# Performance work log

Measured on AMD Instinct MI355X. Metric: run time of the kernel, lower is better.

Reference implementation:

```python
import math
import jax, jax.numpy as jnp
import numpy as np

B, T, D, H, NEXP, TOPK = 2, 1024, 1024, 16, 8, 2
DH = D // H
DFF = 4 * D
NEG = -1e30


def _ln(x, g, b, eps=1e-5):
    m = jnp.mean(x, axis=-1, keepdims=True)
    v = jnp.mean((x - m) ** 2, axis=-1, keepdims=True)
    return (x - m) * jax.lax.rsqrt(v + eps) * g + b


def _build_sin_cos(t, dim, base=10000.0):
    # matches torch build_sin_cos(seq_len, head_dim//2): inv freq over range(0, dim*2, 2)
    pos = jnp.arange(t, dtype=jnp.float32)[:, None]
    inv = jnp.exp(jnp.arange(0, dim * 2, 2, dtype=jnp.float32) * (-math.log(base) / (dim * 2)))
    ang = pos * inv  # (T, dim)
    return jnp.sin(ang), jnp.cos(ang)


def _rope(q, k, sin, cos):
    half = q.shape[-1] // 2
    sin = sin[None, :, None, :]
    cos = cos[None, :, None, :]
    q1, q2 = q[..., :half], q[..., half:]
    k1, k2 = k[..., :half], k[..., half:]
    qr = jnp.concatenate([q1 * cos - q2 * sin, q2 * cos + q1 * sin], axis=-1)
    kr = jnp.concatenate([k1 * cos - k2 * sin, k2 * cos + k1 * sin], axis=-1)
    return qr, kr


def _forward(x, noise, ln1_g, ln1_b, ln2_g, ln2_b, w_qkv, w_proj, w_rl, b_rl, w_rn, b_rn, w1, b1, w2, b2):
    # ---- attention sublayer (LN -> RoPE -> causal attn -> proj, residual) ----
    h = _ln(x, ln1_g, ln1_b)
    qkv = (h @ w_qkv).reshape(B, T, 3, H, DH)
    q, k, v = qkv[:, :, 0], qkv[:, :, 1], qkv[:, :, 2]  # (B,T,H,DH)
    sin, cos = _build_sin_cos(T, DH // 2)
    q, k = _rope(q, k, sin, cos)
    scores = jnp.einsum('bthd,bshd->bhts', q, k) / math.sqrt(DH)
    causal = jnp.tril(jnp.ones((T, T), dtype=bool))
    scores = jnp.where(causal[None, None], scores, NEG)
    attn = jax.nn.softmax(scores, axis=-1)
    ao = jnp.einsum('bhts,bshd->bthd', attn, v).reshape(B, T, D)
    x = x + ao @ w_proj
    # ---- MoE sublayer (noisy top-k router -> capped expert dispatch, residual) ----
    h2 = _ln(x, ln2_g, ln2_b).reshape(B * T, D)
    nz = noise.reshape(B * T, NEXP)
    logits = h2 @ w_rl + b_rl
    noisy = logits + nz * jax.nn.softplus(h2 @ w_rn + b_rn)
    topv, ix = jax.lax.top_k(noisy, TOPK)              # (N,K)
    pk = jax.nn.softmax(topv, axis=-1)                 # softmax over sparse (-inf elsewhere)
    route_p = jnp.sum(pk[..., None] * jax.nn.one_hot(ix, NEXP, dtype=pk.dtype), axis=-2)  # (N,E)
    N = B * T
    cap = int(N * TOPK / NEXP)  # capacity per expert (cap_factor=1.0)
    updates = jnp.zeros((N, D), dtype=x.dtype)
    for i in range(NEXP):
        mask = jnp.any(ix == i, axis=-1)               # (N,) tokens routed to expert i
        sel = jnp.argsort(jnp.logical_not(mask))[:cap]  # first `cap` routed tokens, in order (stable sort)
        valid = mask[sel].astype(x.dtype)              # zero out slots beyond actual routed count
        xe = h2[sel]                                   # (cap, D)
        o = jax.nn.relu(xe @ w1[i] + b1[i]) @ w2[i] + b2[i]
        gate = route_p[sel, i] * valid
        updates = updates.at[sel].add(o * gate[:, None])
    return x + updates.reshape(B, T, D)


def setup_inputs() -> dict:
    key = jax.random.key(0)
    ks = jax.random.split(key, 8)
    s = 0.02
    return {
        'x': jax.random.normal(ks[0], (B, T, D), jnp.float32),
        'noise': jax.random.normal(ks[1], (B, T, NEXP), jnp.float32),
        'ln1_g': jnp.ones((D,), jnp.float32),
        'ln1_b': jnp.zeros((D,), jnp.float32),
        'ln2_g': jnp.ones((D,), jnp.float32),
        'ln2_b': jnp.zeros((D,), jnp.float32),
        'w_qkv': jax.random.normal(ks[2], (D, 3 * D), jnp.float32) * s,
        'w_proj': jax.random.normal(ks[3], (D, D), jnp.float32) * s,
        'w_rl': jax.random.normal(ks[4], (D, NEXP), jnp.float32) * s,
        'b_rl': jnp.zeros((NEXP,), jnp.float32),
        'w_rn': jax.random.normal(ks[5], (D, NEXP), jnp.float32) * s,
        'b_rn': jnp.zeros((NEXP,), jnp.float32),
        'w1': jax.random.normal(ks[6], (NEXP, D, DFF), jnp.float32) * s,
        'b1': jnp.zeros((NEXP, DFF), jnp.float32),
        'w2': jax.random.normal(ks[7], (NEXP, DFF, D), jnp.float32) * s,
        'b2': jnp.zeros((NEXP, D), jnp.float32),
    }


def reference(x, noise, ln1_g, ln1_b, ln2_g, ln2_b, w_qkv, w_proj, w_rl, b_rl, w_rn, b_rn, w1, b1, w2, b2):
    return _forward(x, noise, ln1_g, ln1_b, ln2_g, ln2_b, w_qkv, w_proj, w_rl, b_rl, w_rn, b_rn, w1, b1, w2, b2)
```

## Files before the change

kernel.cpp:

```cpp
#include <hip/hip_runtime.h>


#define TB 1024
#define DD 1024
#define NTOK 2048
#define NEXPERT 8
#define CAPN 512
#define DFF 4096

typedef __attribute__((ext_vector_type(4))) float f32x4;
typedef __attribute__((ext_vector_type(16))) float f32x16;
typedef __attribute__((ext_vector_type(8))) short short8;
typedef __attribute__((ext_vector_type(4))) short short4v;
typedef unsigned short u16;
typedef unsigned int u32;

__device__ __forceinline__ u16 f2bf(float f){
  union { float f; u32 u; } v; v.f = f;
  u32 u = v.u;
  u32 r = (u + 0x7fffu + ((u >> 16) & 1u)) >> 16;
  return (u16)r;
}
__device__ __forceinline__ float bf2f(u16 b){
  union { u32 u; float f; } v; v.u = ((u32)b) << 16;
  return v.f;
}
__device__ __forceinline__ float waveRedSum(float v){
#pragma unroll
  for (int o = 1; o < 64; o <<= 1) v += __shfl_xor(v, o);
  return v;
}

__device__ __forceinline__ void gl16(const u16* g, u16* l){
  __builtin_amdgcn_global_load_lds(
    (const __attribute__((address_space(1))) u32*)g,
    (__attribute__((address_space(3))) u32*)l, 16, 0, 0);
}

__global__ __launch_bounds__(256) void k_prep(
    const float* __restrict__ w_qkv, const float* __restrict__ w_proj,
    const float* __restrict__ w1, const float* __restrict__ w2,
    u16* __restrict__ wqkvT, u16* __restrict__ wprojT,
    u16* __restrict__ w1T, u16* __restrict__ w2T,
    float* __restrict__ st, float* __restrict__ ct)
{
  const int tid = threadIdx.x;
  int bid = blockIdx.x;
  if (bid < 128){
    const int idx = bid * 256 + tid;
    const int t = idx >> 5, i = idx & 31;
    const float inv = expf((float)(2 * i) * (-0.14391157f));
    const float ang = (float)t * inv;
    st[idx] = sinf(ang);
    ct[idx] = cosf(ang);
    return;
  }
  bid -= 128;
  const float* src; u16* dst; int K, N, nx, tile;
  long zoff = 0;
  if (bid < 768){
    src = w_qkv; dst = wqkvT; K = DD; N = 3*DD; nx = 48; tile = bid;
  } else if (bid < 768 + 256){
    src = w_proj; dst = wprojT; K = DD; N = DD; nx = 16; tile = bid - 768;
  } else if (bid < 768 + 256 + 8192){
    const int b2 = bid - (768 + 256);
    src = w1; dst = w1T; K = DD; N = DFF; nx = 64; tile = b2 & 1023;
    zoff = (long)(b2 >> 10) * DD * DFF;
  } else {
    const int b2 = bid - (768 + 256 + 8192);
    src = w2; dst = w2T; K = DFF; N = DD; nx = 16; tile = b2 & 1023;
    zoff = (long)(b2 >> 10) * DFF * DD;
  }
  const int n0 = (tile % nx) * 64, k0 = (tile / nx) * 64;
  __shared__ float tb[64][65];
  const int r  = tid >> 2;
  const int c4 = (tid & 3) * 16;
#pragma unroll
  for (int j = 0; j < 4; ++j){
    const float4 v = *(const float4*)(src + zoff + (long)(k0 + r)*N + n0 + c4 + j*4);
    tb[r][c4 + j*4 + 0] = v.x;
    tb[r][c4 + j*4 + 1] = v.y;
    tb[r][c4 + j*4 + 2] = v.z;
    tb[r][c4 + j*4 + 3] = v.w;
  }
  __syncthreads();
  const int n  = tid >> 2;
  const int ks = (tid & 3) * 16;
  short8 o0, o1;
#pragma unroll
  for (int j = 0; j < 8; ++j){
    o0[j] = (short)f2bf(tb[ks + j][n]);
    o1[j] = (short)f2bf(tb[ks + 8 + j][n]);
  }
  u16* dp = dst + zoff + (long)(n0 + n)*K + k0 + ks;
  *(short8*)dp = o0;
  *(short8*)(dp + 8) = o1;
}

template<bool GATHER>
__device__ __forceinline__ void gemm_core5(
    const u16* __restrict__ A, int lda, const int* __restrict__ rowlist,
    const u16* __restrict__ Bt, int ldb, int K, int kstart, int row0, int col0,
    u16* As0, u16* Bs0, u16* As1, u16* Bs1, f32x16 acc[2][2])
{
  const int tid = threadIdx.x;
  const int lane = tid & 63;
  const int w = tid >> 6;
  const int wr = w >> 1, wc = w & 1;
  const int l31 = lane & 31, l5 = lane >> 5;
  const int rr8 = lane >> 3;
  const int cc8 = ((lane & 7) ^ rr8) * 8;

  const u16* Aq[4];
  const u16* Bq[4];
  int coff[4];
#pragma unroll
  for (int j2 = 0; j2 < 4; ++j2){
    const int j = w + 4*j2;
    long ar;
    if constexpr (GATHER) ar = rowlist[row0 + j*8 + rr8];
    else                  ar = row0 + j*8 + rr8;
    Aq[j2] = A + ar*(long)lda + kstart + cc8;
    Bq[j2] = Bt + (long)(col0 + j*8 + rr8)*ldb + kstart + cc8;
    coff[j2] = j*512;
  }

  const int swz = (l31 & 7) * 8;

#define STAGE5(AS, BS, KOFF) \
  _Pragma("unroll") \
  for (int j2 = 0; j2 < 4; ++j2){ \
    gl16(Aq[j2] + (KOFF), (AS) + coff[j2]); \
    gl16(Bq[j2] + (KOFF), (BS) + coff[j2]); \
  }

#define COMPUTE5(AS, BS) \
  _Pragma("unroll") \
  for (int s = 0; s < 4; ++s){ \
    short8 aF[2], bF[2]; \
    const int cread = ((s*16 + l5*8) ^ swz); \
    _Pragma("unroll") \
    for (int mi = 0; mi < 2; ++mi) \
      aF[mi] = *(const short8*)((AS) + (wr*64 + mi*32 + l31)*64 + cread); \
    _Pragma("unroll") \
    for (int ni = 0; ni < 2; ++ni) \
      bF[ni] = *(const short8*)((BS) + (wc*64 + ni*32 + l31)*64 + cread); \
    _Pragma("unroll") \
    for (int mi = 0; mi < 2; ++mi) \
      _Pragma("unroll") \
      for (int ni = 0; ni < 2; ++ni) \
        acc[mi][ni] = __builtin_amdgcn_mfma_f32_32x32x16_bf16(aF[mi], bF[ni], acc[mi][ni], 0, 0, 0); \
  }

  STAGE5(As0, Bs0, 0)

  for (int k0 = 0; k0 < K; k0 += 128){
    STAGE5(As1, Bs1, k0 + 64)
    asm volatile("s_waitcnt vmcnt(8)" ::: "memory");
    __builtin_amdgcn_s_barrier();
    __builtin_amdgcn_sched_barrier(0);
    COMPUTE5(As0, Bs0)
    __builtin_amdgcn_s_barrier();
    if (k0 + 128 < K){
      STAGE5(As0, Bs0, k0 + 128)
      asm volatile("s_waitcnt vmcnt(8)" ::: "memory");
    } else {
      asm volatile("s_waitcnt vmcnt(0)" ::: "memory");
    }
    __builtin_amdgcn_s_barrier();
    __builtin_amdgcn_sched_barrier(0);
    COMPUTE5(As1, Bs1)
    __builtin_amdgcn_s_barrier();
  }
#undef STAGE5
#undef COMPUTE5
}

#define GEMM_PRE4 \
  __shared__ u16 As0[128*64], Bs0[128*64], As1[128*64], Bs1[128*64]; \
  f32x16 acc[2][2]; \
  _Pragma("unroll") for (int i = 0; i < 2; ++i) \
  _Pragma("unroll") for (int j = 0; j < 2; ++j) \
  _Pragma("unroll") for (int q = 0; q < 16; ++q) acc[i][j][q] = 0.f;

#define GEMM_EPI4_VARS \
  const int lane = threadIdx.x & 63; \
  const int wv = threadIdx.x >> 6;   \
  const int wr = wv >> 1, wc = wv & 1; \
  const int l31 = lane & 31, l5 = lane >> 5;

#define ROW4(mi, r) (row0 + wr*64 + (mi)*32 + ((r)&3) + (((r)>>2)<<3) + l5*4)
#define COL4(ni)    (col0 + wc*64 + (ni)*32 + l31)

__global__ __launch_bounds__(256) void k_ln(const float* __restrict__ x,
    const float* __restrict__ g, const float* __restrict__ bb,
    u16* __restrict__ hb)
{
  const int row = blockIdx.x, tid = threadIdx.x;
  const int w = tid >> 6, lane = tid & 63;
  const float4 xv = *(const float4*)(x + (long)row*DD + tid*4);
  __shared__ float red[8];
  float s = xv.x + xv.y + xv.z + xv.w;
  s = waveRedSum(s);
  if (lane == 0) red[w] = s;
  __syncthreads();
  const float mean = (red[0]+red[1]+red[2]+red[3]) * (1.f/1024.f);
  const float d0 = xv.x-mean, d1 = xv.y-mean, d2 = xv.z-mean, d3 = xv.w-mean;
  float vs = d0*d0 + d1*d1 + d2*d2 + d3*d3;
  vs = waveRedSum(vs);
  if (lane == 0) red[4+w] = vs;
  __syncthreads();
  const float var = (red[4]+red[5]+red[6]+red[7]) * (1.f/1024.f);
  const float inv = rsqrtf(var + 1e-5f);
  const int c = tid*4;
  short4v p;
  p[0] = (short)f2bf(d0*inv*g[c+0] + bb[c+0]);
  p[1] = (short)f2bf(d1*inv*g[c+1] + bb[c+1]);
  p[2] = (short)f2bf(d2*inv*g[c+2] + bb[c+2]);
  p[3] = (short)f2bf(d3*inv*g[c+3] + bb[c+3]);
  *(short4v*)(hb + (long)row*DD + c) = p;
}

__global__ __launch_bounds__(256) void k_gemm_qkv(const u16* __restrict__ h1,
    const u16* __restrict__ wqT, const float* __restrict__ st,
    const float* __restrict__ ct, u16* __restrict__ q_r, u16* __restrict__ k_r,
    u16* __restrict__ v_row)
{
  GEMM_PRE4
  const int id = blockIdx.x;
  const int pcol = id % 24, mt = id / 24;
  const int row0 = mt*128, col0 = pcol*128;
  gemm_core5<false>(h1, DD, nullptr, wqT, DD, DD, 0, row0, col0, As0, Bs0, As1, Bs1, acc);
  GEMM_EPI4_VARS
  if (pcol < 16){
    const int isk = pcol >> 3;
    const int h = (pcol & 7)*2 + wc;
    u16* dstbase = isk ? k_r : q_r;
    const float qs = isk ? 1.f : 0.125f;
#pragma unroll
    for (int mi = 0; mi < 2; ++mi)
#pragma unroll
      for (int r = 0; r < 16; ++r){
        const int rr = ROW4(mi, r);
        const int b = rr >> 10, t = rr & (TB-1);
        const float sv = st[t*32 + l31], cv = ct[t*32 + l31];
        const float a0 = acc[mi][0][r], a1 = acc[mi][1][r];
        const float o1 = (a0*cv - a1*sv) * qs;
        const float o2 = (a1*cv + a0*sv) * qs;
        u16* dst = dstbase + ((long)(b*16 + h)*TB + t)*64 + l31;
        dst[0]  = f2bf(o1);
        dst[32] = f2bf(o2);
      }
  } else {
    const int cb = (pcol - 16)*128 + wc*64;
#pragma unroll
    for (int mi = 0; mi < 2; ++mi)
#pragma unroll
      for (int ni = 0; ni < 2; ++ni)
#pragma unroll
        for (int r = 0; r < 16; ++r){
          const int rr = ROW4(mi, r);
          v_row[(long)rr*DD + cb + ni*32 + l31] = f2bf(acc[mi][ni][r]);
        }
  }
}

__global__ __launch_bounds__(256) void k_vt(const u16* __restrict__ v_row,
    u16* __restrict__ v_t)
{
  __shared__ u16 vt[64*72];
  const int tid = threadIdx.x;
  const int bh = blockIdx.y, b = bh >> 4, h = bh & 15;
  const int t0 = blockIdx.x * 64;
  const int tl = tid >> 2, qq = tid & 3;
  const int t = t0 + tl;
  const long row = (long)(b*TB + t) * DD + h*64;
  const short8 w0 = *(const short8*)(v_row + row + qq*16);
  const short8 w1 = *(const short8*)(v_row + row + qq*16 + 8);
#pragma unroll
  for (int j = 0; j < 8; ++j){
    vt[(qq*16 + j)*72 + tl]     = (u16)w0[j];
    vt[(qq*16 + 8 + j)*72 + tl] = (u16)w1[j];
  }
  __syncthreads();
  const int dh = tid >> 2, seg = tid & 3;
  const short8 r0 = *(const short8*)(vt + dh*72 + seg*16);
  const short8 r1 = *(const short8*)(vt + dh*72 + seg*16 + 8);
  u16* vp = v_t + ((long)bh*64 + dh)*TB + t0 + seg*16;
  *(short8*)vp = r0; *(short8*)(vp + 8) = r1;
}

__global__ __launch_bounds__(512) void k_attn(const u16* __restrict__ q_r,
    const u16* __restrict__ k_r, const u16* __restrict__ v_t,
    u16* __restrict__ aoc, float2* __restrict__ mLc)
{
  const int qt = blockIdx.x, bh = blockIdx.y, ch = blockIdx.z;
  const int kvlen = (qt + 1) * 128;
  const int s_begin = ch * 512;
  if (s_begin >= kvlen) return;
  const int ntile = (min(s_begin + 512, kvlen) - s_begin) >> 6;

  __shared__ u16 K_lds[2][64*64];
  __shared__ u16 V_lds[2][64*64];
  __shared__ u16 P_lds[8][16*80];

  const int tid = threadIdx.x;
  const int w = tid >> 6, lane = tid & 63;
  const int l15 = lane & 15, l4 = lane >> 4;
  const int q0 = qt*128 + w*16;
  u16* P = &P_lds[w][0];

  const int srow = tid >> 3, sslot = tid & 7;
  const u16* kq = k_r + ((long)bh*TB + s_begin + srow)*64 + ((sslot ^ (srow & 7))*8);
  const u16* vq = v_t + ((long)bh*64 + srow)*TB + s_begin + ((sslot ^ (srow & 7))*8);
  u16* kD = &K_lds[0][0] + tid*8;
  u16* vD = &V_lds[0][0] + tid*8;

  const long qoff = ((long)bh*TB + q0 + l15)*64 + l4*8;
  const short8 Qf0 = *(const short8*)(q_r + qoff);
  const short8 Qf1 = *(const short8*)(q_r + qoff + 32);
  const f32x4 fz = {0.f,0.f,0.f,0.f};
  f32x4 O[4];
  float m[4], L[4];
#pragma unroll
  for (int i = 0; i < 4; ++i){ O[i] = fz; m[i] = -1e30f; L[i] = 0.f; }

  gl16(kq, kD);
  gl16(vq, vD);

  for (int t = 0; t < ntile; ++t){
    const int s0 = s_begin + t*64;
    const int cur = t & 1;
    if (t + 1 < ntile){
      gl16(kq + (t+1)*4096, kD + (cur^1)*4096);
      gl16(vq + (t+1)*64,   vD + (cur^1)*4096);
      asm volatile("s_waitcnt vmcnt(2)" ::: "memory");
    } else {
      asm volatile("s_waitcnt vmcnt(0)" ::: "memory");
    }
    __builtin_amdgcn_s_barrier();
    __builtin_amdgcn_sched_barrier(0);
    if (s0 <= q0 + 15){
      const u16* Kb = &K_lds[cur][0];
      const u16* Vb = &V_lds[cur][0];
      f32x4 S[4];
#pragma unroll
      for (int sj = 0; sj < 4; ++sj){
        const int rl = sj*16 + l15;
        const short8 kf0 = *(const short8*)(Kb + rl*64 + ((l4 ^ (rl & 7))*8));
        const short8 kf1 = *(const short8*)(Kb + rl*64 + (((l4 + 4) ^ (rl & 7))*8));
        f32x4 z = fz;
        z = __builtin_amdgcn_mfma_f32_16x16x32_bf16(Qf0, kf0, z, 0, 0, 0);
        z = __builtin_amdgcn_mfma_f32_16x16x32_bf16(Qf1, kf1, z, 0, 0, 0);
        S[sj] = z;
      }
      if (s0 + 63 > q0){
#pragma unroll
        for (int sj = 0; sj < 4; ++sj)
#pragma unroll
          for (int r = 0; r < 4; ++r){
            const int sc = s0 + sj*16 + l15;
            const int qr = q0 + l4*4 + r;
            if (sc > qr) S[sj][r] = -1e30f;
          }
      }
      float vm[4];
#pragma unroll
      for (int r = 0; r < 4; ++r){
        vm[r] = fmaxf(fmaxf(S[0][r], S[1][r]), fmaxf(S[2][r], S[3][r]));
        vm[r] = fmaxf(vm[r], __shfl_xor(vm[r], 1));
        vm[r] = fmaxf(vm[r], __shfl_xor(vm[r], 2));
        vm[r] = fmaxf(vm[r], __shfl_xor(vm[r], 4));
        vm[r] = fmaxf(vm[r], __shfl_xor(vm[r], 8));
      }
      float corr[4], ls[4];
#pragma unroll
      for (int r = 0; r < 4; ++r){
        const float mn = fmaxf(m[r], vm[r]);
        corr[r] = __expf(m[r] - mn);
        m[r] = mn;
        ls[r] = 0.f;
      }
#pragma unroll
      for (int sj = 0; sj < 4; ++sj)
#pragma unroll
        for (int r = 0; r < 4; ++r){
          const float pv = __expf(S[sj][r] - m[r]);
          S[sj][r] = pv;
          ls[r] += pv;
        }
#pragma unroll
      for (int r = 0; r < 4; ++r){
        ls[r] += __shfl_xor(ls[r], 1);
        ls[r] += __shfl_xor(ls[r], 2);
        ls[r] += __shfl_xor(ls[r], 4);
        ls[r] += __shfl_xor(ls[r], 8);
        L[r] = L[r]*corr[r] + ls[r];
      }
#pragma unroll
      for (int nj = 0; nj < 4; ++nj)
#pragma unroll
        for (int r = 0; r < 4; ++r)
          O[nj][r] *= corr[r];
#pragma unroll
      for (int sj = 0; sj < 4; ++sj)
#pragma unroll
        for (int r = 0; r < 4; ++r)
          P[(l4*4 + r)*80 + sj*16 + l15] = f2bf(S[sj][r]);
      asm volatile("s_waitcnt lgkmcnt(0)" ::: "memory");
      __builtin_amdgcn_sched_barrier(0);
      const short8 pf0 = *(const short8*)(P + l15*80 + l4*8);
      const short8 pf1 = *(const short8*)(P + l15*80 + 32 + l4*8);
#pragma unroll
      for (int nj = 0; nj < 4; ++nj){
        const int rl = nj*16 + l15;
        const short8 vf0 = *(const short8*)(Vb + rl*64 + ((l4 ^ (rl & 7))*8));
        const short8 vf1 = *(const short8*)(Vb + rl*64 + (((l4 + 4) ^ (rl & 7))*8));
        O[nj] = __builtin_amdgcn_mfma_f32_16x16x32_bf16(pf0, vf0, O[nj], 0, 0, 0);
        O[nj] = __builtin_amdgcn_mfma_f32_16x16x32_bf16(pf1, vf1, O[nj], 0, 0, 0);
      }
    }
    __builtin_amdgcn_sched_barrier(0);
    __builtin_amdgcn_s_barrier();
  }
  const long obase = ((long)(bh*8 + qt)*2 + ch) * 8192;
#pragma unroll
  for (int nj = 0; nj < 4; ++nj)
#pragma unroll
    for (int r = 0; r < 4; ++r)
      aoc[obase + (long)(w*16 + l4*4 + r)*64 + nj*16 + l15] = f2bf(O[nj][r]);
  if (l15 == 0){
#pragma unroll
    for (int r = 0; r < 4; ++r)
      mLc[((long)(bh*8 + qt)*2 + ch)*128 + w*16 + l4*4 + r] = make_float2(m[r], L[r]);
  }
}

__global__ __launch_bounds__(256) void k_attn_comb(const u16* __restrict__ aoc,
    const float2* __restrict__ mLc, u16* __restrict__ ao)
{
  const int bq = blockIdx.x;
  const int qt = bq & 7, bh = bq >> 3, b = bh >> 4, h = bh & 15;
  const int nc2 = (qt >= 4);
  const int d = threadIdx.x & 63;
  const int r0 = threadIdx.x >> 6;
  const long base = (long)bq * 2 * 8192;
  const long mbase = (long)bq * 2 * 128;
  for (int rp = 0; rp < 32; ++rp){
    const int r = rp*4 + r0;
    const float2 ml0 = mLc[mbase + r];
    float o, Lg;
    if (nc2){
      const float2 ml1 = mLc[mbase + 128 + r];
      const float mg = fmaxf(ml0.x, ml1.x);
      const float w0 = __expf(ml0.x - mg), w1 = __expf(ml1.x - mg);
      o  = w0 * bf2f(aoc[base + (long)r*64 + d]) + w1 * bf2f(aoc[base + 8192 + (long)r*64 + d]);
      Lg = w0 * ml0.y + w1 * ml1.y;
    } else {
      o  = bf2f(aoc[base + (long)r*64 + d]);
      Lg = ml0.y;
    }
    const int t = qt*128 + r;
    ao[((long)b*TB + t)*DD + h*64 + d] = f2bf(o / Lg);
  }
}

__global__ __launch_bounds__(256) void k_gemm_proj(const u16* __restrict__ ao,
    const u16* __restrict__ wpT, const float* __restrict__ x, float* __restrict__ out)
{
  GEMM_PRE4
  const int id = blockIdx.x;
  const int pcol = id % 8, mt = id / 8;
  const int row0 = mt*128, col0 = pcol*128;
  gemm_core5<false>(ao, DD, nullptr, wpT, DD, DD, 0, row0, col0, As0, Bs0, As1, Bs1, acc);
  GEMM_EPI4_VARS
#pragma unroll
  for (int mi = 0; mi < 2; ++mi)
#pragma unroll
    for (int ni = 0; ni < 2; ++ni)
#pragma unroll
      for (int r = 0; r < 16; ++r){
        const int rr = ROW4(mi, r);
        const int cc = COL4(ni);
        out[(long)rr*DD + cc] = x[(long)rr*DD + cc] + acc[mi][ni][r];
      }
}

__global__ __launch_bounds__(256) void k_ln2r(const float* __restrict__ x,
    const float* __restrict__ g, const float* __restrict__ bb,
    const float* __restrict__ w_rl, const float* __restrict__ b_rl,
    const float* __restrict__ w_rn, const float* __restrict__ b_rn,
    const float* __restrict__ noise, u16* __restrict__ h2b,
    int2* __restrict__ tok_e, float2* __restrict__ tok_g, int* __restrict__ slot_of)
{
  const int row = blockIdx.x, tid = threadIdx.x;
  const int w = tid >> 6, lane = tid & 63;
  const float4 xv = *(const float4*)(x + (long)row*DD + tid*4);
  __shared__ float red[8];
  __shared__ float red2[4][16];
  float s = xv.x + xv.y + xv.z + xv.w;
  s = waveRedSum(s);
  if (lane == 0) red[w] = s;
  __syncthreads();
  const float mean = (red[0]+red[1]+red[2]+red[3]) * (1.f/1024.f);
  const float d0 = xv.x-mean, d1 = xv.y-mean, d2 = xv.z-mean, d3 = xv.w-mean;
  float vs = d0*d0 + d1*d1 + d2*d2 + d3*d3;
  vs = waveRedSum(vs);
  if (lane == 0) red[4+w] = vs;
  __syncthreads();
  const float var = (red[4]+red[5]+red[6]+red[7]) * (1.f/1024.f);
  const float inv = rsqrtf(var + 1e-5f);
  const int c = tid*4;
  const float hv[4] = {
    d0*inv*g[c+0] + bb[c+0], d1*inv*g[c+1] + bb[c+1],
    d2*inv*g[c+2] + bb[c+2], d3*inv*g[c+3] + bb[c+3]};
  short4v p;
#pragma unroll
  for (int j = 0; j < 4; ++j) p[j] = (short)f2bf(hv[j]);
  *(short4v*)(h2b + (long)row*DD + c) = p;

  float accl[8] = {0,0,0,0,0,0,0,0};
  float accn[8] = {0,0,0,0,0,0,0,0};
#pragma unroll
  for (int j = 0; j < 4; ++j){
    const int k = c + j;
    const float4 a = *(const float4*)(w_rl + k*8);
    const float4 b = *(const float4*)(w_rl + k*8 + 4);
    accl[0] += hv[j]*a.x; accl[1] += hv[j]*a.y; accl[2] += hv[j]*a.z; accl[3] += hv[j]*a.w;
    accl[4] += hv[j]*b.x; accl[5] += hv[j]*b.y; accl[6] += hv[j]*b.z; accl[7] += hv[j]*b.w;
    const float4 cc = *(const float4*)(w_rn + k*8);
    const float4 d = *(const float4*)(w_rn + k*8 + 4);
    accn[0] += hv[j]*cc.x; accn[1] += hv[j]*cc.y; accn[2] += hv[j]*cc.z; accn[3] += hv[j]*cc.w;
    accn[4] += hv[j]*d.x; accn[5] += hv[j]*d.y; accn[6] += hv[j]*d.z; accn[7] += hv[j]*d.w;
  }
#pragma unroll
  for (int e = 0; e < 8; ++e){ accl[e] = waveRedSum(accl[e]); accn[e] = waveRedSum(accn[e]); }
  if (lane == 0){
#pragma unroll
    for (int e = 0; e < 8; ++e){ red2[w][e] = accl[e]; red2[w][8+e] = accn[e]; }
  }
  __syncthreads();
  if (tid == 0){
    float nv[8];
#pragma unroll
    for (int e = 0; e < 8; ++e){
      const float lr = red2[0][e]+red2[1][e]+red2[2][e]+red2[3][e] + b_rl[e];
      const float lnv = red2[0][8+e]+red2[1][8+e]+red2[2][8+e]+red2[3][8+e] + b_rn[e];
      const float sp = fmaxf(lnv, 0.f) + log1pf(expf(-fabsf(lnv)));
      nv[e] = lr + noise[row*8 + e] * sp;
    }
    int bi = 0; float bvv = nv[0];
#pragma unroll
    for (int e = 1; e < 8; ++e) if (nv[e] > bvv){ bvv = nv[e]; bi = e; }
    int si = (bi == 0) ? 1 : 0;
    float sv = nv[si];
#pragma unroll
    for (int e = 0; e < 8; ++e) if (e != bi && nv[e] > sv){ sv = nv[e]; si = e; }
    const float tt = expf(sv - bvv);
    tok_e[row] = make_int2(bi, si);
    tok_g[row] = make_float2(1.f/(1.f + tt), tt/(1.f + tt));
    slot_of[row*2]     = -1;
    slot_of[row*2 + 1] = -1;
  }
}

__global__ __launch_bounds__(256) void k_assign(const int2* __restrict__ tok_e,
    int* __restrict__ expert_tok, int* __restrict__ slot_of)
{
  const int e = blockIdx.x, tid = threadIdx.x;
  __shared__ int cnt[256];
  expert_tok[e*CAPN + tid] = 0;
  expert_tok[e*CAPN + 256 + tid] = 0;
  int which[8]; int c = 0;
  const int t0 = tid * 8;
#pragma unroll
  for (int j = 0; j < 8; ++j){
    const int2 te = tok_e[t0 + j];
    int wj = -1;
    if (te.x == e) wj = 0; else if (te.y == e) wj = 1;
    which[j] = wj;
    c += (wj >= 0) ? 1 : 0;
  }
  cnt[tid] = c;
  __syncthreads();
  if (tid == 0){
    int run = 0;
    for (int i = 0; i < 256; ++i){ const int v = cnt[i]; cnt[i] = run; run += v; }
  }
  __syncthreads();
  int pos = cnt[tid];
#pragma unroll
  for (int j = 0; j < 8; ++j){
    if (which[j] >= 0){
      if (pos < CAPN){
        expert_tok[e*CAPN + pos] = t0 + j;
        slot_of[(t0 + j)*2 + which[j]] = e*CAPN + pos;
      }
      ++pos;
    }
  }
}

__global__ __launch_bounds__(256) void k_ffn1(const u16* __restrict__ h2b,
    const u16* __restrict__ w1T, const float* __restrict__ b1,
    const int* __restrict__ expert_tok, u16* __restrict__ act)
{
  GEMM_PRE4
  const int id = blockIdx.x;
  const int chunk = (id & 7) * 128 + (id >> 3);
  const int mt = chunk & 3, pcol = (chunk >> 2) & 31, z = chunk >> 7;
  const int row0 = mt*128, col0 = pcol*128;
  gemm_core5<true>(h2b, DD, expert_tok + z*CAPN, w1T + (long)z*DD*DFF, DD, DD, 0,
                   row0, col0, As0, Bs0, As1, Bs1, acc);
  GEMM_EPI4_VARS
#pragma unroll
  for (int mi = 0; mi < 2; ++mi)
#pragma unroll
    for (int ni = 0; ni < 2; ++ni)
#pragma unroll
      for (int r = 0; r < 16; ++r){
        const int rr = ROW4(mi, r);
        const int cc = COL4(ni);
        const float val = fmaxf(acc[mi][ni][r] + b1[z*DFF + cc], 0.f);
        act[((long)z*CAPN + rr)*DFF + cc] = f2bf(val);
      }
}

__global__ __launch_bounds__(256) void k_ffn2(const u16* __restrict__ act,
    const u16* __restrict__ w2T, float* __restrict__ partial)
{
  GEMM_PRE4
  const int id = blockIdx.x;
  const int chunk = (id & 7) * 64 + (id >> 3);
  const int ks = chunk & 1, mt = (chunk >> 1) & 3, pcol = (chunk >> 3) & 7, z = chunk >> 6;
  const int row0 = mt*128, col0 = pcol*128;
  gemm_core5<false>(act + (long)z*CAPN*DFF, DFF, nullptr,
                    w2T + (long)z*DFF*DD, DFF, 2048, ks*2048,
                    row0, col0, As0, Bs0, As1, Bs1, acc);
  GEMM_EPI4_VARS
  float* pp = partial + (long)ks*NEXPERT*CAPN*DD;
#pragma unroll
  for (int mi = 0; mi < 2; ++mi)
#pragma unroll
    for (int ni = 0; ni < 2; ++ni)
#pragma unroll
      for (int r = 0; r < 16; ++r){
        const int rr = ROW4(mi, r);
        const int cc = COL4(ni);
        pp[((long)z*CAPN + rr)*DD + cc] = acc[mi][ni][r];
      }
}

__global__ __launch_bounds__(256) void k_combine(float* __restrict__ out,
    const int* __restrict__ slot_of, const float2* __restrict__ tok_g,
    const float* __restrict__ partial, const float* __restrict__ b2)
{
  const int tok = blockIdx.x, c = threadIdx.x * 4;
  float4 o = *(float4*)(out + (long)tok*DD + c);
  const int2 ss = *(const int2*)(slot_of + tok*2);
  const float2 g = tok_g[tok];
#pragma unroll
  for (int j = 0; j < 2; ++j){
    const int s = j ? ss.y : ss.x;
    const float gw = j ? g.y : g.x;
    if (s >= 0){
      const int e = s >> 9;
      float4 a = *(const float4*)(b2 + e*DD + c);
#pragma unroll
      for (int ks = 0; ks < 2; ++ks){
        const float4 pv = *(const float4*)(partial + (long)ks*NEXPERT*CAPN*DD + (long)s*DD + c);
        a.x += pv.x; a.y += pv.y; a.z += pv.z; a.w += pv.w;
      }
      o.x += gw*a.x; o.y += gw*a.y; o.z += gw*a.z; o.w += gw*a.w;
    }
  }
  *(float4*)(out + (long)tok*DD + c) = o;
}

extern "C" void kernel_launch(void* const* d_in, const int* in_sizes, int n_in,
                              void* d_out, int out_size, void* d_ws, size_t ws_size,
                              hipStream_t stream)
{
  (void)in_sizes; (void)n_in; (void)out_size; (void)ws_size;
  const float* x      = (const float*)d_in[0];
  const float* noise  = (const float*)d_in[1];
  const float* ln1_g  = (const float*)d_in[2];
  const float* ln1_b  = (const float*)d_in[3];
  const float* ln2_g  = (const float*)d_in[4];
  const float* ln2_b  = (const float*)d_in[5];
  const float* w_qkv  = (const float*)d_in[6];
  const float* w_proj = (const float*)d_in[7];
  const float* w_rl   = (const float*)d_in[8];
  const float* b_rl   = (const float*)d_in[9];
  const float* w_rn   = (const float*)d_in[10];
  const float* b_rn   = (const float*)d_in[11];
  const float* w1     = (const float*)d_in[12];
  const float* b1     = (const float*)d_in[13];
  const float* w2     = (const float*)d_in[14];
  const float* b2     = (const float*)d_in[15];
  float* out = (float*)d_out;

  char* p = (char*)d_ws;
  auto carve = [&](size_t bytes) -> void* {
    void* r = (void*)p;
    p += (bytes + 255) & ~(size_t)255;
    return r;
  };
  const size_t SLOT = (size_t)NTOK*DD*2;
  float* sin_t      = (float*)carve((size_t)TB*32*4);
  float* cos_t      = (float*)carve((size_t)TB*32*4);
  char*  region     = (char*)carve(SLOT*8);
  u16*   h1    = (u16*)region;
  u16*   v_row = (u16*)(region + SLOT);
  u16*   q_r   = (u16*)(region + SLOT*4);
  u16*   k_r   = (u16*)(region + SLOT*5);
  u16*   v_t   = (u16*)(region + SLOT*6);
  u16*   ao    = (u16*)(region + SLOT*7);
  u16*   aoc   = (u16*)region;
  float2* mLc  = (float2*)(region + SLOT*2);
  u16*   act   = (u16*)region;
  u16*   h2b        = (u16*)  carve((size_t)NTOK*DD*2);
  int2*  tok_e      = (int2*) carve((size_t)NTOK*8);
  float2* tok_g     = (float2*)carve((size_t)NTOK*8);
  int*   slot_of    = (int*)  carve((size_t)NTOK*2*4);
  int*   expert_tok = (int*)  carve((size_t)NEXPERT*CAPN*4);
  u16*   wqkvT      = (u16*)  carve((size_t)DD*3*DD*2);
  u16*   wprojT     = (u16*)  carve((size_t)DD*DD*2);
  u16*   w1T        = (u16*)  carve((size_t)NEXPERT*DD*DFF*2);
  u16*   w2T        = (u16*)  carve((size_t)NEXPERT*DFF*DD*2);
  float* partial    = (float*)w1T;

  k_prep   <<<17536, 256, 0, stream>>>(w_qkv, w_proj, w1, w2,
                                       wqkvT, wprojT, w1T, w2T, sin_t, cos_t);
  k_ln     <<<NTOK, 256, 0, stream>>>(x, ln1_g, ln1_b, h1);
  k_gemm_qkv<<<384, 256, 0, stream>>>(h1, wqkvT, sin_t, cos_t, q_r, k_r, v_row);
  k_vt     <<<dim3(16, 32), 256, 0, stream>>>(v_row, v_t);
  k_attn   <<<dim3(8, 32, 2), 512, 0, stream>>>(q_r, k_r, v_t, aoc, mLc);
  k_attn_comb<<<256, 256, 0, stream>>>(aoc, mLc, ao);
  k_gemm_proj<<<128, 256, 0, stream>>>(ao, wprojT, x, out);
  k_ln2r   <<<NTOK, 256, 0, stream>>>(out, ln2_g, ln2_b, w_rl, b_rl, w_rn, b_rn,
                                      noise, h2b, tok_e, tok_g, slot_of);
  k_assign <<<NEXPERT, 256, 0, stream>>>(tok_e, expert_tok, slot_of);
  k_ffn1   <<<1024, 256, 0, stream>>>(h2b, w1T, b1, expert_tok, act);
  k_ffn2   <<<512, 256, 0, stream>>>(act, w2T, partial);
  k_combine<<<NTOK, 256, 0, stream>>>(out, slot_of, tok_g, partial, b2);
}
```

Baseline: 325.5 us.

## Fuse fp32 weight transpose and bf16 conversion into GEMM B-tile loading

Drops the separate prep kernel that transposed every fp32 weight into bf16 scratch buffers. The GEMMs now read fp32 weights directly from global memory into registers, pack them to bf16 with v_cvt_pk_bf16_f32, and write them into swizzled LDS tiles on a 64-wide K pipeline. This removes one full read-convert-write pass over roughly 300MB of weights. In exchange the GEMMs load twice as many bytes for B, and B staging goes through registers instead of direct global-to-LDS loads.

```diff
diff --git a/kernel.cpp b/kernel.cpp
--- a/kernel.cpp
+++ b/kernel.cpp
@@ -25,6 +25,11 @@
   union { u32 u; float f; } v; v.u = ((u32)b) << 16;
   return v.f;
 }
+__device__ __forceinline__ u32 cvtpk(float lo, float hi){
+  u32 r;
+  asm("v_cvt_pk_bf16_f32 %0, %1, %2" : "=v"(r) : "v"(lo), "v"(hi));
+  return r;
+}
 __device__ __forceinline__ float waveRedSum(float v){
 #pragma unroll
   for (int o = 1; o < 64; o <<= 1) v += __shfl_xor(v, o);
@@ -37,70 +42,19 @@
     (__attribute__((address_space(3))) u32*)l, 16, 0, 0);
 }
 
-__global__ __launch_bounds__(256) void k_prep(
-    const float* __restrict__ w_qkv, const float* __restrict__ w_proj,
-    const float* __restrict__ w1, const float* __restrict__ w2,
-    u16* __restrict__ wqkvT, u16* __restrict__ wprojT,
-    u16* __restrict__ w1T, u16* __restrict__ w2T,
-    float* __restrict__ st, float* __restrict__ ct)
-{
-  const int tid = threadIdx.x;
-  int bid = blockIdx.x;
-  if (bid < 128){
-    const int idx = bid * 256 + tid;
-    const int t = idx >> 5, i = idx & 31;
-    const float inv = expf((float)(2 * i) * (-0.14391157f));
-    const float ang = (float)t * inv;
-    st[idx] = sinf(ang);
-    ct[idx] = cosf(ang);
-    return;
-  }
-  bid -= 128;
-  const float* src; u16* dst; int K, N, nx, tile;
-  long zoff = 0;
-  if (bid < 768){
-    src = w_qkv; dst = wqkvT; K = DD; N = 3*DD; nx = 48; tile = bid;
-  } else if (bid < 768 + 256){
-    src = w_proj; dst = wprojT; K = DD; N = DD; nx = 16; tile = bid - 768;
-  } else if (bid < 768 + 256 + 8192){
-    const int b2 = bid - (768 + 256);
-    src = w1; dst = w1T; K = DD; N = DFF; nx = 64; tile = b2 & 1023;
-    zoff = (long)(b2 >> 10) * DD * DFF;
-  } else {
-    const int b2 = bid - (768 + 256 + 8192);
-    src = w2; dst = w2T; K = DFF; N = DD; nx = 16; tile = b2 & 1023;
-    zoff = (long)(b2 >> 10) * DFF * DD;
-  }
-  const int n0 = (tile % nx) * 64, k0 = (tile / nx) * 64;
-  __shared__ float tb[64][65];
-  const int r  = tid >> 2;
-  const int c4 = (tid & 3) * 16;
-#pragma unroll
-  for (int j = 0; j < 4; ++j){
-    const float4 v = *(const float4*)(src + zoff + (long)(k0 + r)*N + n0 + c4 + j*4);
-    tb[r][c4 + j*4 + 0] = v.x;
-    tb[r][c4 + j*4 + 1] = v.y;
-    tb[r][c4 + j*4 + 2] = v.z;
-    tb[r][c4 + j*4 + 3] = v.w;
-  }
-  __syncthreads();
-  const int n  = tid >> 2;
-  const int ks = (tid & 3) * 16;
-  short8 o0, o1;
-#pragma unroll
-  for (int j = 0; j < 8; ++j){
-    o0[j] = (short)f2bf(tb[ks + j][n]);
-    o1[j] = (short)f2bf(tb[ks + 8 + j][n]);
-  }
-  u16* dp = dst + zoff + (long)(n0 + n)*K + k0 + ks;
-  *(short8*)dp = o0;
-  *(short8*)(dp + 8) = o1;
+__global__ __launch_bounds__(256) void k_sincos(float* __restrict__ st, float* __restrict__ ct){
+  const int idx = blockIdx.x * 256 + threadIdx.x;
+  const int t = idx >> 5, i = idx & 31;
+  const float inv = expf((float)(2 * i) * (-0.14391157f));
+  const float ang = (float)t * inv;
+  st[idx] = sinf(ang);
+  ct[idx] = cosf(ang);
 }
 
 template<bool GATHER>
-__device__ __forceinline__ void gemm_core5(
+__device__ __forceinline__ void gemm_core6(
     const u16* __restrict__ A, int lda, const int* __restrict__ rowlist,
-    const u16* __restrict__ Bt, int ldb, int K, int kstart, int row0, int col0,
+    const float* __restrict__ Bf, int ldb, int K, int kstart, int row0, int col0,
     u16* As0, u16* Bs0, u16* As1, u16* Bs1, f32x16 acc[2][2])
 {
   const int tid = threadIdx.x;
@@ -112,7 +66,6 @@
   const int cc8 = ((lane & 7) ^ rr8) * 8;
 
   const u16* Aq[4];
-  const u16* Bq[4];
   int coff[4];
 #pragma unroll
   for (int j2 = 0; j2 < 4; ++j2){
@@ -121,20 +74,36 @@
     if constexpr (GATHER) ar = rowlist[row0 + j*8 + rr8];
     else                  ar = row0 + j*8 + rr8;
     Aq[j2] = A + ar*(long)lda + kstart + cc8;
-    Bq[j2] = Bt + (long)(col0 + j*8 + rr8)*ldb + kstart + cc8;
     coff[j2] = j*512;
   }
 
+  const int bkg = lane & 7;
+  const int bn4 = w*32 + ((lane >> 3) & 7)*4;
+  const float* Bq = Bf + (long)(kstart + bkg*8)*ldb + col0 + bn4;
+  f32x4 bv[8];
+
   const int swz = (l31 & 7) * 8;
 
-#define STAGE5(AS, BS, KOFF) \
+#define STAGEA(AS, KOFF) \
   _Pragma("unroll") \
-  for (int j2 = 0; j2 < 4; ++j2){ \
-    gl16(Aq[j2] + (KOFF), (AS) + coff[j2]); \
-    gl16(Bq[j2] + (KOFF), (BS) + coff[j2]); \
-  }
-
-#define COMPUTE5(AS, BS) \
+  for (int j2 = 0; j2 < 4; ++j2) gl16(Aq[j2] + (KOFF), (AS) + coff[j2]);
+
+#define BLOAD(KOFF) \
+  _Pragma("unroll") \
+  for (int r = 0; r < 8; ++r) bv[r] = *(const f32x4*)(Bq + (long)((KOFF) + r)*ldb);
+
+#define BWRITE(BS) \
+  _Pragma("unroll") \
+  for (int j = 0; j < 4; ++j){ \
+    const int n = bn4 + j; \
+    const u32 p0 = cvtpk(bv[0][j], bv[1][j]); \
+    const u32 p1 = cvtpk(bv[2][j], bv[3][j]); \
+    const u32 p2 = cvtpk(bv[4][j], bv[5][j]); \
+    const u32 p3 = cvtpk(bv[6][j], bv[7][j]); \
+    *(uint4*)((BS) + n*64 + ((bkg*8) ^ ((n & 7)*8))) = make_uint4(p0, p1, p2, p3); \
+  }
+
+#define COMPUTE6(AS, BS) \
   _Pragma("unroll") \
   for (int s = 0; s < 4; ++s){ \
     short8 aF[2], bF[2]; \
@@ -152,28 +121,41 @@
         acc[mi][ni] = __builtin_amdgcn_mfma_f32_32x32x16_bf16(aF[mi], bF[ni], acc[mi][ni], 0, 0, 0); \
   }
 
-  STAGE5(As0, Bs0, 0)
-
-  for (int k0 = 0; k0 < K; k0 += 128){
-    STAGE5(As1, Bs1, k0 + 64)
-    asm volatile("s_waitcnt vmcnt(8)" ::: "memory");
-    __builtin_amdgcn_s_barrier();
-    __builtin_amdgcn_sched_barrier(0);
-    COMPUTE5(As0, Bs0)
-    __builtin_amdgcn_s_barrier();
-    if (k0 + 128 < K){
-      STAGE5(As0, Bs0, k0 + 128)
-      asm volatile("s_waitcnt vmcnt(8)" ::: "memory");
+  const int nt = K >> 6;
+  BLOAD(0)
+  STAGEA(As0, 0)
+  asm volatile("s_waitcnt vmcnt(4)" ::: "memory");
+  BWRITE(Bs0)
+  asm volatile("s_waitcnt lgkmcnt(0)" ::: "memory");
+  __builtin_amdgcn_s_barrier();
+
+  u16* Ac = As0; u16* Bc = Bs0; u16* An = As1; u16* Bn = Bs1;
+  for (int t = 0; t < nt; ++t){
+    const bool more = (t + 1 < nt);
+    if (more){
+      BLOAD((t + 1) << 6)
+      STAGEA(An, (t + 1) << 6)
+      asm volatile("s_waitcnt vmcnt(12)" ::: "memory");
     } else {
       asm volatile("s_waitcnt vmcnt(0)" ::: "memory");
     }
     __builtin_amdgcn_s_barrier();
     __builtin_amdgcn_sched_barrier(0);
-    COMPUTE5(As1, Bs1)
+    COMPUTE6(Ac, Bc)
+    if (more){
+      asm volatile("s_waitcnt vmcnt(4)" ::: "memory");
+      BWRITE(Bn)
+      asm volatile("s_waitcnt lgkmcnt(0)" ::: "memory");
+    }
     __builtin_amdgcn_s_barrier();
-  }
-#undef STAGE5
-#undef COMPUTE5
+    u16* tmp;
+    tmp = Ac; Ac = An; An = tmp;
+    tmp = Bc; Bc = Bn; Bn = tmp;
+  }
+#undef STAGEA
+#undef BLOAD
+#undef BWRITE
+#undef COMPUTE6
 }
 
 #define GEMM_PRE4 \
@@ -222,7 +204,7 @@
 }
 
 __global__ __launch_bounds__(256) void k_gemm_qkv(const u16* __restrict__ h1,
-    const u16* __restrict__ wqT, const float* __restrict__ st,
+    const float* __restrict__ wq, const float* __restrict__ st,
     const float* __restrict__ ct, u16* __restrict__ q_r, u16* __restrict__ k_r,
     u16* __restrict__ v_row)
 {
@@ -230,7 +212,7 @@
   const int id = blockIdx.x;
   const int pcol = id % 24, mt = id / 24;
   const int row0 = mt*128, col0 = pcol*128;
-  gemm_core5<false>(h1, DD, nullptr, wqT, DD, DD, 0, row0, col0, As0, Bs0, As1, Bs1, acc);
+  gemm_core6<false>(h1, DD, nullptr, wq, 3*DD, DD, 0, row0, col0, As0, Bs0, As1, Bs1, acc);
   GEMM_EPI4_VARS
   if (pcol < 16){
     const int isk = pcol >> 3;
@@ -466,13 +448,13 @@
 }
 
 __global__ __launch_bounds__(256) void k_gemm_proj(const u16* __restrict__ ao,
-    const u16* __restrict__ wpT, const float* __restrict__ x, float* __restrict__ out)
+    const float* __restrict__ wp, const float* __restrict__ x, float* __restrict__ out)
 {
   GEMM_PRE4
   const int id = blockIdx.x;
   const int pcol = id % 8, mt = id / 8;
   const int row0 = mt*128, col0 = pcol*128;
-  gemm_core5<false>(ao, DD, nullptr, wpT, DD, DD, 0, row0, col0, As0, Bs0, As1, Bs1, acc);
+  gemm_core6<false>(ao, DD, nullptr, wp, DD, DD, 0, row0, col0, As0, Bs0, As1, Bs1, acc);
   GEMM_EPI4_VARS
 #pragma unroll
   for (int mi = 0; mi < 2; ++mi)
@@ -602,7 +584,7 @@
 }
 
 __global__ __launch_bounds__(256) void k_ffn1(const u16* __restrict__ h2b,
-    const u16* __restrict__ w1T, const float* __restrict__ b1,
+    const float* __restrict__ w1, const float* __restrict__ b1,
     const int* __restrict__ expert_tok, u16* __restrict__ act)
 {
   GEMM_PRE4
@@ -610,7 +592,7 @@
   const int chunk = (id & 7) * 128 + (id >> 3);
   const int mt = chunk & 3, pcol = (chunk >> 2) & 31, z = chunk >> 7;
   const int row0 = mt*128, col0 = pcol*128;
-  gemm_core5<true>(h2b, DD, expert_tok + z*CAPN, w1T + (long)z*DD*DFF, DD, DD, 0,
+  gemm_core6<true>(h2b, DD, expert_tok + z*CAPN, w1 + (long)z*DD*DFF, DFF, DD, 0,
                    row0, col0, As0, Bs0, As1, Bs1, acc);
   GEMM_EPI4_VARS
 #pragma unroll
@@ -627,15 +609,15 @@
 }
 
 __global__ __launch_bounds__(256) void k_ffn2(const u16* __restrict__ act,
-    const u16* __restrict__ w2T, float* __restrict__ partial)
+    const float* __restrict__ w2, float* __restrict__ partial)
 {
   GEMM_PRE4
   const int id = blockIdx.x;
   const int chunk = (id & 7) * 64 + (id >> 3);
   const int ks = chunk & 1, mt = (chunk >> 1) & 3, pcol = (chunk >> 3) & 7, z = chunk >> 6;
   const int row0 = mt*128, col0 = pcol*128;
-  gemm_core5<false>(act + (long)z*CAPN*DFF, DFF, nullptr,
-                    w2T + (long)z*DFF*DD, DFF, 2048, ks*2048,
+  gemm_core6<false>(act + (long)z*CAPN*DFF, DFF, nullptr,
+                    w2 + (long)z*DFF*DD, DD, 2048, ks*2048,
                     row0, col0, As0, Bs0, As1, Bs1, acc);
   GEMM_EPI4_VARS
   float* pp = partial + (long)ks*NEXPERT*CAPN*DD;
@@ -724,24 +706,19 @@
   float2* tok_g     = (float2*)carve((size_t)NTOK*8);
   int*   slot_of    = (int*)  carve((size_t)NTOK*2*4);
   int*   expert_tok = (int*)  carve((size_t)NEXPERT*CAPN*4);
-  u16*   wqkvT      = (u16*)  carve((size_t)DD*3*DD*2);
-  u16*   wprojT     = (u16*)  carve((size_t)DD*DD*2);
-  u16*   w1T        = (u16*)  carve((size_t)NEXPERT*DD*DFF*2);
-  u16*   w2T        = (u16*)  carve((size_t)NEXPERT*DFF*DD*2);
-  float* partial    = (float*)w1T;
-
-  k_prep   <<<17536, 256, 0, stream>>>(w_qkv, w_proj, w1, w2,
-                                       wqkvT, wprojT, w1T, w2T, sin_t, cos_t);
+  float* partial    = (float*)carve((size_t)2*NEXPERT*CAPN*DD*4);
+
+  k_sincos <<<128, 256, 0, stream>>>(sin_t, cos_t);
   k_ln     <<<NTOK, 256, 0, stream>>>(x, ln1_g, ln1_b, h1);
-  k_gemm_qkv<<<384, 256, 0, stream>>>(h1, wqkvT, sin_t, cos_t, q_r, k_r, v_row);
+  k_gemm_qkv<<<384, 256, 0, stream>>>(h1, w_qkv, sin_t, cos_t, q_r, k_r, v_row);
   k_vt     <<<dim3(16, 32), 256, 0, stream>>>(v_row, v_t);
   k_attn   <<<dim3(8, 32, 2), 512, 0, stream>>>(q_r, k_r, v_t, aoc, mLc);
   k_attn_comb<<<256, 256, 0, stream>>>(aoc, mLc, ao);
-  k_gemm_proj<<<128, 256, 0, stream>>>(ao, wprojT, x, out);
+  k_gemm_proj<<<128, 256, 0, stream>>>(ao, w_proj, x, out);
   k_ln2r   <<<NTOK, 256, 0, stream>>>(out, ln2_g, ln2_b, w_rl, b_rl, w_rn, b_rn,
                                       noise, h2b, tok_e, tok_g, slot_of);
   k_assign <<<NEXPERT, 256, 0, stream>>>(tok_e, expert_tok, slot_of);
-  k_ffn1   <<<1024, 256, 0, stream>>>(h2b, w1T, b1, expert_tok, act);
-  k_ffn2   <<<512, 256, 0, stream>>>(act, w2T, partial);
+  k_ffn1   <<<1024, 256, 0, stream>>>(h2b, w1, b1, expert_tok, act);
+  k_ffn2   <<<512, 256, 0, stream>>>(act, w2, partial);
   k_combine<<<NTOK, 256, 0, stream>>>(out, slot_of, tok_g, partial, b2);
 }
```

Measured after the change: 344.3 us. +5.8%, slower.
